# Kernel optimization log

Measured on AMD Instinct MI355X. Metric: run time of the kernel, lower is better.

The kernel has to match this reference:

```python
import jax, jax.numpy as jnp
import numpy as np

B, N = 128, 4096
D_WHAT = 64
NEG_FRAC = 0.1
EPS = 1e-3


def setup_inputs() -> dict:
    rng = np.random.RandomState(0)
    # per-row present counts, deterministic, max = 256 -> static n_objects
    counts = 200 + (np.arange(B) % 57)  # max = 200 + 56 = 256
    max_present = int(counts.max())
    n_objects = max_present + int(NEG_FRAC * N)  # 256 + 409 = 665
    # random present positions per row: rank of a random matrix
    prio = rng.rand(B, N)
    rank = np.argsort(np.argsort(prio, axis=1), axis=1)
    present = (rank < counts[:, None]).astype(np.float32)  # [B, N]
    z_present = jnp.asarray(present[..., None])  # [B, N, 1], values in {0, 1}

    key = jax.random.key(0)
    k = jax.random.split(key, 6)
    return {
        "z_where": jax.random.uniform(k[0], (B, N, 4), dtype=jnp.float32),
        "z_present": z_present,
        "z_what_loc": jax.random.normal(k[1], (B, N, D_WHAT), dtype=jnp.float32),
        "z_what_scale": jax.random.uniform(k[2], (B, N, D_WHAT), dtype=jnp.float32) + 0.1,
        "z_depth_loc": jax.random.normal(k[3], (B, N, 1), dtype=jnp.float32),
        "z_depth_scale": jax.random.uniform(k[4], (B, N, 1), dtype=jnp.float32) + 0.1,
        "neg_priority": jax.random.uniform(k[5], (B, N), dtype=jnp.float32),
        "n_objects": n_objects,
    }


def reference(z_where, z_present, z_what_loc, z_what_scale,
              z_depth_loc, z_depth_scale, neg_priority, n_objects):
    # --- reset_non_present: latents with z_present <= eps get (loc=0, scale=1) ---
    mask = z_present > EPS  # [B, N, 1], broadcasts over feature dim
    z_what_loc = jnp.where(mask, z_what_loc, 0.0)
    z_what_scale = jnp.where(mask, z_what_scale, 1.0)
    z_depth_loc = jnp.where(mask, z_depth_loc, 0.0)
    z_depth_scale = jnp.where(mask, z_depth_scale, 1.0)

    # --- convert_to_square: wh -> max(w, h) for both dims ---
    wh_idx = jnp.argmax(z_where[..., 2:], axis=-1) + 2  # [B, N]
    m = jnp.take_along_axis(z_where, wh_idx[..., None], axis=-1)  # [B, N, 1]
    z_where_sq = jnp.concatenate([z_where[..., :2], m, m], axis=-1)  # [B, N, 4]

    # representation fns: where_fn/present_fn = identity, what_fn/depth_fn = loc
    zp = z_present  # [B, N, 1]

    # --- add_negative: mark (n_objects - n_present) random absent slots with -1 ---
    n_present = jnp.sum(zp[..., 0], axis=1).astype(jnp.int32)  # [B]
    zero_mask = zp[..., 0] == 0  # [B, N]
    prio = jnp.where(zero_mask, neg_priority, jnp.inf)
    rank = jnp.argsort(jnp.argsort(prio, axis=1), axis=1)  # per-row rank of priorities
    n_neg = n_objects - n_present  # [B]
    neg_mask = zero_mask & (rank < n_neg[:, None])  # [B, N]
    modified = jnp.where(neg_mask[..., None], -1.0, zp)  # [B, N, 1]

    # --- filter_representation: keep slots with modified != 0, exactly n_objects/row ---
    present_mask = modified[..., 0] != 0  # [B, N], exactly n_objects True per row
    # stable argsort on ~mask puts True slots first, preserving original order
    idx = jnp.argsort(~present_mask, axis=1, stable=True)[:, :n_objects]  # [B, K]
    gather = lambda t: jnp.take_along_axis(t, idx[..., None], axis=1)

    return (gather(z_where_sq),   # [B, K, 4]
            gather(modified),     # [B, K, 1]
            gather(z_what_loc),   # [B, K, 64]
            gather(z_depth_loc))  # [B, K, 1]
```

## Files before the change

### kernel.cpp

```cpp
#include <hip/hip_runtime.h>
#include <stdint.h>

typedef unsigned int   u32;
typedef unsigned long long u64;

#define Bb   128
#define Nn   4096
#define DW   64
#define TPB  256
#define PERT (Nn / TPB)
#define NBINS 4096
#define LCAP 512
#define CCAP 1024
#define BPR  8

template<bool DO_COPY>
__global__ __launch_bounds__(TPB) void sel_kernel(
    const float* __restrict__ zwhere, const float* __restrict__ zpres,
    const float* __restrict__ zwhat,  const float* __restrict__ zdepth,
    const float* __restrict__ nprio,
    float* __restrict__ out0, float* __restrict__ out1,
    float* __restrict__ out2, float* __restrict__ out3,
    int* __restrict__ srcws, int K)
{
    __shared__ float prio[Nn];
    __shared__ u32   hist[NBINS];
    __shared__ u64   blist[LCAP];
    __shared__ int   compact[CCAP];
    __shared__ u64   presb[Nn / 64];
    __shared__ int   cnt[TPB];
    __shared__ int   s_np, s_m, s_bstar, s_cbefore;
    __shared__ u64   s_thr;

    const int b   = blockIdx.x;
    const int tid = threadIdx.x;

    for (int i = tid; i < NBINS; i += TPB) hist[i] = 0;
    for (int i = tid; i < Nn / 64; i += TPB) presb[i] = 0;
    if (tid == 0) { s_np = 0; s_m = 0; s_bstar = -1; s_cbefore = 0; s_thr = 0; }
    __syncthreads();

    int myp = 0;
    for (int i = tid; i < Nn; i += TPB) {
        float z = zpres[(size_t)b * Nn + i];
        float p = nprio[(size_t)b * Nn + i];
        prio[i] = p;
        if (z != 0.0f) {
            myp++;
            atomicOr(&presb[i >> 6], 1ull << (i & 63));
        } else {
            int bin = (int)(p * (float)NBINS);
            bin = bin < 0 ? 0 : (bin > NBINS - 1 ? NBINS - 1 : bin);
            atomicAdd(&hist[bin], 1u);
        }
    }
    atomicAdd(&s_np, myp);
    __syncthreads();

    const int n_neg = K - s_np;

    int hl = 0;
    #pragma unroll
    for (int j = 0; j < NBINS / TPB; j++) hl += (int)hist[tid * (NBINS / TPB) + j];
    cnt[tid] = hl;
    __syncthreads();
    for (int d = 1; d < TPB; d <<= 1) {
        int v = (tid >= d) ? cnt[tid - d] : 0;
        __syncthreads();
        cnt[tid] += v;
        __syncthreads();
    }
    {
        int hincl = cnt[tid];
        int hbase = hincl - hl;
        if (n_neg > hbase && n_neg <= hincl) {
            int c = hbase;
            for (int j = 0; j < NBINS / TPB; j++) {
                int h = (int)hist[tid * (NBINS / TPB) + j];
                if (n_neg <= c + h) { s_bstar = tid * (NBINS / TPB) + j; s_cbefore = c; break; }
                c += h;
            }
        }
    }
    __syncthreads();
    const int bstar = s_bstar;
    const int r     = n_neg - s_cbefore;

    for (int i = tid; i < Nn; i += TPB) {
        if (!((presb[i >> 6] >> (i & 63)) & 1ull)) {
            int bin = (int)(prio[i] * (float)NBINS);
            bin = bin < 0 ? 0 : (bin > NBINS - 1 ? NBINS - 1 : bin);
            if (bin == bstar) {
                int pos = atomicAdd(&s_m, 1);
                if (pos < LCAP)
                    blist[pos] = (((u64)__float_as_uint(prio[i])) << 12) | (u64)i;
            }
        }
    }
    __syncthreads();
    int m = s_m; if (m > LCAP) m = LCAP;
    for (int j = tid; j < m; j += TPB) {
        u64 kj = blist[j];
        int rank = 0;
        for (int l = 0; l < m; l++) rank += (blist[l] < kj) ? 1 : 0;
        if (rank == r - 1) s_thr = kj;
    }
    __syncthreads();
    const u64 thr = s_thr;

    int lc = 0;
    u32 selbits = 0, negbits = 0;
    const int base_n = tid * PERT;
    #pragma unroll
    for (int j = 0; j < PERT; j++) {
        int n = base_n + j;
        bool present = (presb[n >> 6] >> (n & 63)) & 1ull;
        bool neg = false;
        if (!present) {
            int bin = (int)(prio[n] * (float)NBINS);
            bin = bin < 0 ? 0 : (bin > NBINS - 1 ? NBINS - 1 : bin);
            u64 key = (((u64)__float_as_uint(prio[n])) << 12) | (u64)n;
            neg = (bin < bstar) || (bin == bstar && key <= thr);
        }
        if (present || neg) { selbits |= (1u << j); lc++; }
        if (neg) negbits |= (1u << j);
    }
    cnt[tid] = lc;
    __syncthreads();
    for (int d = 1; d < TPB; d <<= 1) {
        int v = (tid >= d) ? cnt[tid - d] : 0;
        __syncthreads();
        cnt[tid] += v;
        __syncthreads();
    }
    int pos = cnt[tid] - lc;
    #pragma unroll
    for (int j = 0; j < PERT; j++) {
        if (selbits & (1u << j)) {
            int n = base_n + j;
            bool neg = (negbits >> j) & 1;
            if (pos < CCAP && pos < K) {
                compact[pos] = n | (neg ? (1 << 30) : 0);
                out1[(size_t)b * K + pos] = neg ? -1.0f : 1.0f;
            }
            pos++;
        }
    }
    __syncthreads();

    if (!DO_COPY) {
        for (int k = tid; k < K; k += TPB)
            srcws[(size_t)b * K + k] = compact[k];
        return;
    }

    for (int i = tid; i < K * 16; i += TPB) {
        int k = i >> 4, lane = i & 15;
        int e = compact[k];
        int src = e & (Nn - 1);
        bool neg = (e >> 30) & 1;
        float4 v = make_float4(0.f, 0.f, 0.f, 0.f);
        if (!neg) v = *(const float4*)(zwhat + ((size_t)(b * Nn + src) * DW + lane * 4));
        *(float4*)(out2 + ((size_t)(b * K + k) * DW + lane * 4)) = v;
    }
    for (int k = tid; k < K; k += TPB) {
        int e = compact[k];
        int src = e & (Nn - 1);
        bool neg = (e >> 30) & 1;
        float4 w = *(const float4*)(zwhere + (size_t)(b * Nn + src) * 4);
        float mv = (w.z >= w.w) ? w.z : w.w;
        float4 o; o.x = w.x; o.y = w.y; o.z = mv; o.w = mv;
        *(float4*)(out0 + (size_t)(b * K + k) * 4) = o;
        out3[(size_t)b * K + k] = neg ? 0.0f : zdepth[(size_t)b * Nn + src];
    }
}

__global__ __launch_bounds__(TPB) void copy_kernel(
    const float* __restrict__ zwhere, const float* __restrict__ zwhat,
    const float* __restrict__ zdepth, const int* __restrict__ srcws,
    float* __restrict__ out0, float* __restrict__ out2, float* __restrict__ out3,
    int K, int spb)
{
    int b = blockIdx.x / BPR;
    int chunk = blockIdx.x % BPR;
    int k0 = chunk * spb;
    int k1 = k0 + spb; if (k1 > K) k1 = K;
    int tid = threadIdx.x;

    for (int i = k0 * 16 + tid; i < k1 * 16; i += TPB) {
        int k = i >> 4, lane = i & 15;
        int e = srcws[(size_t)b * K + k];
        int src = e & (Nn - 1);
        bool neg = (e >> 30) & 1;
        float4 v = make_float4(0.f, 0.f, 0.f, 0.f);
        if (!neg) v = *(const float4*)(zwhat + ((size_t)(b * Nn + src) * DW + lane * 4));
        *(float4*)(out2 + ((size_t)(b * K + k) * DW + lane * 4)) = v;
    }
    for (int k = k0 + tid; k < k1; k += TPB) {
        int e = srcws[(size_t)b * K + k];
        int src = e & (Nn - 1);
        bool neg = (e >> 30) & 1;
        float4 w = *(const float4*)(zwhere + (size_t)(b * Nn + src) * 4);
        float mv = (w.z >= w.w) ? w.z : w.w;
        float4 o; o.x = w.x; o.y = w.y; o.z = mv; o.w = mv;
        *(float4*)(out0 + (size_t)(b * K + k) * 4) = o;
        out3[(size_t)b * K + k] = neg ? 0.0f : zdepth[(size_t)b * Nn + src];
    }
}

extern "C" void kernel_launch(void* const* d_in, const int* in_sizes, int n_in,
                              void* d_out, int out_size, void* d_ws, size_t ws_size,
                              hipStream_t stream) {
    const float* zwhere = (const float*)d_in[0];
    const float* zpres  = (const float*)d_in[1];
    const float* zwhat  = (const float*)d_in[2];
    const float* zdepth = (const float*)d_in[4];
    const float* nprio  = (const float*)d_in[6];
    int K = out_size / (Bb * 70);

    float* out  = (float*)d_out;
    float* out0 = out;
    float* out1 = out0 + (size_t)Bb * K * 4;
    float* out2 = out1 + (size_t)Bb * K;
    float* out3 = out2 + (size_t)Bb * K * DW;

    size_t need = (size_t)Bb * K * sizeof(int);
    if (ws_size >= need) {
        int* srcws = (int*)d_ws;
        sel_kernel<false><<<Bb, TPB, 0, stream>>>(zwhere, zpres, zwhat, zdepth, nprio,
                                                  out0, out1, out2, out3, srcws, K);
        int spb = (K + BPR - 1) / BPR;
        copy_kernel<<<Bb * BPR, TPB, 0, stream>>>(zwhere, zwhat, zdepth, srcws,
                                                  out0, out2, out3, K, spb);
    } else {
        sel_kernel<true><<<Bb, TPB, 0, stream>>>(zwhere, zpres, zwhat, zdepth, nprio,
                                                 out0, out1, out2, out3, nullptr, K);
    }
}
```

Baseline: 262.2 us.

## Keep priorities in registers, use wave-shuffle scans, move out1 writes to copy

Each thread now loads its 16 contiguous presence and priority values with float4 loads and keeps them in registers. This replaces the shared prio array and the atomicOr presence bitmask. The two Hillis-Steele shared-memory prefix scans become wave-shuffle scans combined across waves with one barrier, which cuts many __syncthreads. Present counts are reduced per wave before the atomic, and the out1 writes move into the copy pass so they are coalesced. Less shared memory may allow more blocks per CU, but there is only one block per row (128 blocks).

```diff
diff --git a/kernel.cpp b/kernel.cpp
--- a/kernel.cpp
+++ b/kernel.cpp
@@ -8,11 +8,33 @@
 #define Nn   4096
 #define DW   64
 #define TPB  256
-#define PERT (Nn / TPB)
+#define PERT 16
 #define NBINS 4096
 #define LCAP 512
 #define CCAP 1024
 #define BPR  8
+
+__device__ __forceinline__ int wave_iscan(int v) {
+    int lane = threadIdx.x & 63;
+    #pragma unroll
+    for (int d = 1; d < 64; d <<= 1) {
+        int u = __shfl_up(v, d, 64);
+        v += (lane >= d) ? u : 0;
+    }
+    return v;
+}
+
+__device__ __forceinline__ int block_escan(int v, int* wsum) {
+    int tid  = threadIdx.x;
+    int wid  = tid >> 6;
+    int incl = wave_iscan(v);
+    if ((tid & 63) == 63) wsum[wid] = incl;
+    __syncthreads();
+    int base = 0;
+    #pragma unroll
+    for (int w = 0; w < TPB / 64; w++) base += (w < wid) ? wsum[w] : 0;
+    return base + incl - v;
+}
 
 template<bool DO_COPY>
 __global__ __launch_bounds__(TPB) void sel_kernel(
@@ -23,126 +45,117 @@
     float* __restrict__ out2, float* __restrict__ out3,
     int* __restrict__ srcws, int K)
 {
-    __shared__ float prio[Nn];
-    __shared__ u32   hist[NBINS];
-    __shared__ u64   blist[LCAP];
-    __shared__ int   compact[CCAP];
-    __shared__ u64   presb[Nn / 64];
-    __shared__ int   cnt[TPB];
-    __shared__ int   s_np, s_m, s_bstar, s_cbefore;
-    __shared__ u64   s_thr;
+    __shared__ u32 hist[NBINS];
+    __shared__ u64 blist[LCAP];
+    __shared__ int compact[CCAP];
+    __shared__ int wsumA[4], wsumB[4];
+    __shared__ int s_m, s_bstar, s_cbefore, s_np;
+    __shared__ u64 s_thr;
 
     const int b   = blockIdx.x;
     const int tid = threadIdx.x;
 
     for (int i = tid; i < NBINS; i += TPB) hist[i] = 0;
-    for (int i = tid; i < Nn / 64; i += TPB) presb[i] = 0;
-    if (tid == 0) { s_np = 0; s_m = 0; s_bstar = -1; s_cbefore = 0; s_thr = 0; }
-    __syncthreads();
-
-    int myp = 0;
-    for (int i = tid; i < Nn; i += TPB) {
-        float z = zpres[(size_t)b * Nn + i];
-        float p = nprio[(size_t)b * Nn + i];
-        prio[i] = p;
-        if (z != 0.0f) {
-            myp++;
-            atomicOr(&presb[i >> 6], 1ull << (i & 63));
-        } else {
-            int bin = (int)(p * (float)NBINS);
+    if (tid == 0) { s_m = 0; s_bstar = -1; s_cbefore = 0; s_np = 0; s_thr = 0; }
+
+    float p[PERT];
+    u32 pm = 0;
+    {
+        const float4* zp4 = (const float4*)(zpres + (size_t)b * Nn);
+        const float4* pr4 = (const float4*)(nprio + (size_t)b * Nn);
+        #pragma unroll
+        for (int q = 0; q < 4; q++) {
+            float4 z  = zp4[tid * 4 + q];
+            float4 pp = pr4[tid * 4 + q];
+            p[4*q+0] = pp.x; p[4*q+1] = pp.y; p[4*q+2] = pp.z; p[4*q+3] = pp.w;
+            if (z.x != 0.0f) pm |= 1u << (4*q+0);
+            if (z.y != 0.0f) pm |= 1u << (4*q+1);
+            if (z.z != 0.0f) pm |= 1u << (4*q+2);
+            if (z.w != 0.0f) pm |= 1u << (4*q+3);
+        }
+    }
+    __syncthreads();
+
+    #pragma unroll
+    for (int j = 0; j < PERT; j++) {
+        if (!((pm >> j) & 1u)) {
+            int bin = (int)(p[j] * (float)NBINS);
             bin = bin < 0 ? 0 : (bin > NBINS - 1 ? NBINS - 1 : bin);
             atomicAdd(&hist[bin], 1u);
         }
     }
-    atomicAdd(&s_np, myp);
+    {
+        int myp = __popc(pm);
+        #pragma unroll
+        for (int d = 32; d >= 1; d >>= 1) myp += __shfl_down(myp, d, 64);
+        if ((tid & 63) == 0) atomicAdd(&s_np, myp);
+    }
     __syncthreads();
 
     const int n_neg = K - s_np;
 
     int hl = 0;
     #pragma unroll
-    for (int j = 0; j < NBINS / TPB; j++) hl += (int)hist[tid * (NBINS / TPB) + j];
-    cnt[tid] = hl;
-    __syncthreads();
-    for (int d = 1; d < TPB; d <<= 1) {
-        int v = (tid >= d) ? cnt[tid - d] : 0;
-        __syncthreads();
-        cnt[tid] += v;
-        __syncthreads();
-    }
-    {
-        int hincl = cnt[tid];
-        int hbase = hincl - hl;
-        if (n_neg > hbase && n_neg <= hincl) {
-            int c = hbase;
-            for (int j = 0; j < NBINS / TPB; j++) {
-                int h = (int)hist[tid * (NBINS / TPB) + j];
-                if (n_neg <= c + h) { s_bstar = tid * (NBINS / TPB) + j; s_cbefore = c; break; }
-                c += h;
-            }
+    for (int j = 0; j < 16; j++) hl += (int)hist[tid * 16 + j];
+    int hbase = block_escan(hl, wsumA);
+    if (n_neg > hbase && n_neg <= hbase + hl) {
+        int c = hbase;
+        for (int j = 0; j < 16; j++) {
+            int h = (int)hist[tid * 16 + j];
+            if (n_neg <= c + h) { s_bstar = tid * 16 + j; s_cbefore = c; break; }
+            c += h;
         }
     }
     __syncthreads();
     const int bstar = s_bstar;
     const int r     = n_neg - s_cbefore;
 
-    for (int i = tid; i < Nn; i += TPB) {
-        if (!((presb[i >> 6] >> (i & 63)) & 1ull)) {
-            int bin = (int)(prio[i] * (float)NBINS);
+    #pragma unroll
+    for (int j = 0; j < PERT; j++) {
+        if (!((pm >> j) & 1u)) {
+            int bin = (int)(p[j] * (float)NBINS);
             bin = bin < 0 ? 0 : (bin > NBINS - 1 ? NBINS - 1 : bin);
             if (bin == bstar) {
                 int pos = atomicAdd(&s_m, 1);
                 if (pos < LCAP)
-                    blist[pos] = (((u64)__float_as_uint(prio[i])) << 12) | (u64)i;
+                    blist[pos] = (((u64)__float_as_uint(p[j])) << 12) | (u64)(tid * PERT + j);
             }
         }
     }
     __syncthreads();
-    int m = s_m; if (m > LCAP) m = LCAP;
-    for (int j = tid; j < m; j += TPB) {
-        u64 kj = blist[j];
-        int rank = 0;
-        for (int l = 0; l < m; l++) rank += (blist[l] < kj) ? 1 : 0;
-        if (rank == r - 1) s_thr = kj;
+    {
+        int m = s_m; if (m > LCAP) m = LCAP;
+        for (int j2 = tid; j2 < m; j2 += TPB) {
+            u64 kj = blist[j2];
+            int rank = 0;
+            for (int l = 0; l < m; l++) rank += (blist[l] < kj) ? 1 : 0;
+            if (rank == r - 1) s_thr = kj;
+        }
     }
     __syncthreads();
     const u64 thr = s_thr;
 
+    u32 selbits = 0, negbits = 0;
     int lc = 0;
-    u32 selbits = 0, negbits = 0;
-    const int base_n = tid * PERT;
-    #pragma unroll
-    for (int j = 0; j < PERT; j++) {
-        int n = base_n + j;
-        bool present = (presb[n >> 6] >> (n & 63)) & 1ull;
+    #pragma unroll
+    for (int j = 0; j < PERT; j++) {
+        bool present = (pm >> j) & 1u;
         bool neg = false;
         if (!present) {
-            int bin = (int)(prio[n] * (float)NBINS);
+            int bin = (int)(p[j] * (float)NBINS);
             bin = bin < 0 ? 0 : (bin > NBINS - 1 ? NBINS - 1 : bin);
-            u64 key = (((u64)__float_as_uint(prio[n])) << 12) | (u64)n;
+            u64 key = (((u64)__float_as_uint(p[j])) << 12) | (u64)(tid * PERT + j);
             neg = (bin < bstar) || (bin == bstar && key <= thr);
         }
-        if (present || neg) { selbits |= (1u << j); lc++; }
-        if (neg) negbits |= (1u << j);
-    }
-    cnt[tid] = lc;
-    __syncthreads();
-    for (int d = 1; d < TPB; d <<= 1) {
-        int v = (tid >= d) ? cnt[tid - d] : 0;
-        __syncthreads();
-        cnt[tid] += v;
-        __syncthreads();
-    }
-    int pos = cnt[tid] - lc;
-    #pragma unroll
-    for (int j = 0; j < PERT; j++) {
-        if (selbits & (1u << j)) {
-            int n = base_n + j;
-            bool neg = (negbits >> j) & 1;
-            if (pos < CCAP && pos < K) {
-                compact[pos] = n | (neg ? (1 << 30) : 0);
-                out1[(size_t)b * K + pos] = neg ? -1.0f : 1.0f;
-            }
+        if (present || neg) { selbits |= 1u << j; lc++; }
+        if (neg) negbits |= 1u << j;
+    }
+    int pos = block_escan(lc, wsumB);
+    #pragma unroll
+    for (int j = 0; j < PERT; j++) {
+        if ((selbits >> j) & 1u) {
+            if (pos < CCAP)
+                compact[pos] = (tid * PERT + j) | ((((negbits >> j) & 1u)) << 30);
             pos++;
         }
     }
@@ -171,6 +184,7 @@
         float mv = (w.z >= w.w) ? w.z : w.w;
         float4 o; o.x = w.x; o.y = w.y; o.z = mv; o.w = mv;
         *(float4*)(out0 + (size_t)(b * K + k) * 4) = o;
+        out1[(size_t)b * K + k] = neg ? -1.0f : 1.0f;
         out3[(size_t)b * K + k] = neg ? 0.0f : zdepth[(size_t)b * Nn + src];
     }
 }
@@ -178,10 +192,11 @@
 __global__ __launch_bounds__(TPB) void copy_kernel(
     const float* __restrict__ zwhere, const float* __restrict__ zwhat,
     const float* __restrict__ zdepth, const int* __restrict__ srcws,
-    float* __restrict__ out0, float* __restrict__ out2, float* __restrict__ out3,
+    float* __restrict__ out0, float* __restrict__ out1,
+    float* __restrict__ out2, float* __restrict__ out3,
     int K, int spb)
 {
-    int b = blockIdx.x / BPR;
+    int b     = blockIdx.x / BPR;
     int chunk = blockIdx.x % BPR;
     int k0 = chunk * spb;
     int k1 = k0 + spb; if (k1 > K) k1 = K;
@@ -204,6 +219,7 @@
         float mv = (w.z >= w.w) ? w.z : w.w;
         float4 o; o.x = w.x; o.y = w.y; o.z = mv; o.w = mv;
         *(float4*)(out0 + (size_t)(b * K + k) * 4) = o;
+        out1[(size_t)b * K + k] = neg ? -1.0f : 1.0f;
         out3[(size_t)b * K + k] = neg ? 0.0f : zdepth[(size_t)b * Nn + src];
     }
 }
@@ -231,7 +247,7 @@
                                                   out0, out1, out2, out3, srcws, K);
         int spb = (K + BPR - 1) / BPR;
         copy_kernel<<<Bb * BPR, TPB, 0, stream>>>(zwhere, zwhat, zdepth, srcws,
-                                                  out0, out2, out3, K, spb);
+                                                  out0, out1, out2, out3, K, spb);
     } else {
         sel_kernel<true><<<Bb, TPB, 0, stream>>>(zwhere, zpres, zwhat, zdepth, nprio,
                                                  out0, out1, out2, out3, nullptr, K);
```

After: 253.2 us. 3.4% less time.
